# Performance work log

Hardware: AMD Instinct MI355X
Metric: run time of the kernel (lower is better)

Reference implementation:

```python
import jax, jax.numpy as jnp
import numpy as np


def setup_inputs() -> dict:
    key = jax.random.key(0)
    ks = jax.random.split(key, 12)
    B, S, D, HS, O = 512, 128, 128, 256, 1
    stdv = 1.0 / np.sqrt(HS)
    u = lambda k, shp: jax.random.uniform(k, shp, jnp.float32, -stdv, stdv)
    return {
        "H": jax.random.normal(ks[0], (B, S, D), jnp.float32),
        "y0": jax.random.normal(ks[1], (B, O), jnp.float32),
        "Wa": u(ks[2], (D, S)),
        "Ua": u(ks[3], (HS, S)),
        "ba": u(ks[4], (S,)),
        "Va": u(ks[5], (S, S)),
        "W": u(ks[6], (D, 4 * HS)),
        "U": u(ks[7], (HS, 4 * HS)),
        "bias": u(ks[8], (4 * HS,)),
        "Wy": u(ks[9], (O, 4 * HS)),
        "fc_W": u(ks[10], (O, HS)),
        "fc_b": u(ks[11], (O,)),
    }


def reference(H, y0, Wa, Ua, ba, Va, W, U, bias, Wy, fc_W, fc_b):
    B, S, D = H.shape
    HS = U.shape[0]
    # s_t in the original is initialized to zeros and never updated, so the
    # s_t @ Ua term is a constant zero; kept explicitly for faithfulness.
    s0 = jnp.zeros((B, HS), H.dtype)
    sUa = s0 @ Ua  # [B, S], zeros
    h0 = jnp.zeros((B, HS), H.dtype)
    c0 = jnp.zeros((B, HS), H.dtype)

    def step(carry, h_t):  # h_t: [B, D] = H[:, t, :]
        h_prev, c_prev, y_prev = carry
        logits = jnp.tanh(h_t @ Wa + sUa + ba) @ Va          # [B, S]
        beta = jax.nn.softmax(logits, axis=1)                # [B, S]
        pooled = jnp.einsum('bs,bsd->bd', beta, H)           # attention pool over full seq
        gates = pooled @ W + h_prev @ U + y_prev @ Wy + bias # [B, 4*HS]
        i_t, f_t, g_t, o_t = jnp.split(gates, 4, axis=1)
        c_new = jax.nn.sigmoid(f_t) * c_prev + jax.nn.sigmoid(i_t) * jnp.tanh(g_t)
        h_new = jax.nn.sigmoid(o_t) * jnp.tanh(c_new)
        y_new = h_new @ fc_W.T + fc_b                        # [B, O]
        return (h_new, c_new, y_new), h_new

    xs = jnp.transpose(H, (1, 0, 2))  # [S, B, D]
    (h_f, c_f, y_f), seq = jax.lax.scan(step, (h0, c0, y0), xs)
    hidden_seq = jnp.transpose(seq, (1, 0, 2))  # [B, S, HS]
    return y_f, hidden_seq
```

## Files before the change

### kernel.cpp

```cpp
#include <hip/hip_runtime.h>
#include <hip/hip_bf16.h>


using bf16x8 = __attribute__((ext_vector_type(8))) short;
using f32x4  = __attribute__((ext_vector_type(4))) float;

#define DEV static __device__ __forceinline__

DEV unsigned short f2bf(float x) {
    unsigned u = __float_as_uint(x);
    u += 0x7fffu + ((u >> 16) & 1u);
    return (unsigned short)(u >> 16);
}
DEV float bf2f(unsigned short s) { return __uint_as_float(((unsigned)s) << 16); }
DEV float sigm(float x) { return 1.0f / (1.0f + __expf(-x)); }
DEV float tanh_f(float x) { float e = __expf(2.0f * x); return 1.0f - 2.0f / (e + 1.0f); }
DEV f32x4 mfma16(bf16x8 a, bf16x8 b, f32x4 c) {
    return __builtin_amdgcn_mfma_f32_16x16x32_bf16(a, b, c, 0, 0, 0);
}

DEV void stage128(const unsigned short* __restrict__ src, unsigned short* dst, int rows, int tid) {
    int chunks = rows * 16;
    for (int i = tid; i < chunks; i += 256) {
        int r = i >> 4, c = (i & 15) << 3;
        *(bf16x8*)(dst + r * 136 + c) = *(const bf16x8*)(src + r * 128 + c);
    }
}
DEV void stage128f(const float* __restrict__ src, unsigned short* dst, int rows, int tid) {
    int chunks = rows * 16;
    for (int i = tid; i < chunks; i += 256) {
        int r = i >> 4, c = (i & 15) << 3;
        const float* s = src + r * 128 + c;
        bf16x8 o;
        #pragma unroll
        for (int e = 0; e < 8; ++e) o[e] = (short)f2bf(s[e]);
        *(bf16x8*)(dst + r * 136 + c) = o;
    }
}

__global__ void k_prepw(const float* __restrict__ Wa, const float* __restrict__ Va,
                        const float* __restrict__ W, const float* __restrict__ U,
                        const float* __restrict__ fcW, const float* __restrict__ Wy,
                        unsigned short* __restrict__ WaT, unsigned short* __restrict__ VaT,
                        unsigned short* __restrict__ WT, unsigned short* __restrict__ Upk) {
    int idx = blockIdx.x * 256 + threadIdx.x;
    if (idx < 16384) {
        int n = idx >> 7, k = idx & 127;
        WaT[idx] = f2bf(Wa[k * 128 + n]);
    } else if (idx < 32768) {
        int i = idx - 16384;
        int n = i >> 7, k = i & 127;
        VaT[i] = f2bf(Va[k * 128 + n]);
    } else if (idx < 163840) {
        int i = idx - 32768;
        int n = i >> 7, k = i & 127;
        WT[i] = f2bf(W[k * 1024 + n]);
    } else if (idx < 425984) {
        int i = idx - 163840;
        int j = i & 7, ll = (i >> 3) & 63, tt = (i >> 9) & 7, kc = (i >> 12) & 7, w = i >> 15;
        int k = kc * 32 + (ll >> 4) * 8 + j;
        int n = (tt >> 1) * 256 + w * 32 + (tt & 1) * 16 + (ll & 15);
        Upk[i] = f2bf(U[k * 1024 + n] + fcW[k] * Wy[n]);
    }
}

__global__ __launch_bounds__(256) void k_prept(const float* __restrict__ H,
                                               unsigned short* __restrict__ HT) {
    __shared__ unsigned short tl[128 * 130];
    int b = blockIdx.x, tid = threadIdx.x;
    const float* Hb = H + (size_t)b * 16384;
    for (int i = tid; i < 16384; i += 256) {
        int s = i >> 7, d = i & 127;
        tl[s * 130 + d] = f2bf(Hb[i]);
    }
    __syncthreads();
    unsigned short* HTb = HT + (size_t)b * 16384;
    for (int i = tid; i < 16384; i += 256) {
        int d = i >> 7, s = i & 127;
        HTb[i] = tl[s * 130 + d];
    }
}

__global__ __launch_bounds__(256) void k_att(const float* __restrict__ H,
                                             const unsigned short* __restrict__ WaT,
                                             const unsigned short* __restrict__ VaT,
                                             const unsigned short* __restrict__ HT,
                                             const float* __restrict__ ba,
                                             unsigned short* __restrict__ poolT) {
    __shared__ unsigned short A1[128 * 136];
    __shared__ unsigned short B1[128 * 136];
    int tid = threadIdx.x, b = blockIdx.x;
    int w = tid >> 6, l = tid & 63, q = l >> 4, r = l & 15;

    stage128f(H + (size_t)b * 16384, A1, 128, tid);
    stage128(WaT, B1, 128, tid);
    __syncthreads();
    f32x4 acc[2][8] = {};
    #pragma unroll
    for (int kc = 0; kc < 4; ++kc)
        #pragma unroll
        for (int mt = 0; mt < 2; ++mt) {
            bf16x8 a = *(const bf16x8*)(A1 + (w * 32 + mt * 16 + r) * 136 + kc * 32 + q * 8);
            #pragma unroll
            for (int nt = 0; nt < 8; ++nt) {
                bf16x8 bb = *(const bf16x8*)(B1 + (nt * 16 + r) * 136 + kc * 32 + q * 8);
                acc[mt][nt] = mfma16(a, bb, acc[mt][nt]);
            }
        }
    __syncthreads();
    #pragma unroll
    for (int nt = 0; nt < 8; ++nt) {
        float bav = ba[nt * 16 + r];
        #pragma unroll
        for (int mt = 0; mt < 2; ++mt)
            #pragma unroll
            for (int j = 0; j < 4; ++j)
                B1[(w * 32 + mt * 16 + q * 4 + j) * 136 + nt * 16 + r] =
                    f2bf(tanh_f(acc[mt][nt][j] + bav));
    }
    stage128(VaT, A1, 128, tid);
    __syncthreads();

    f32x4 lacc[2][8] = {};
    #pragma unroll
    for (int kc = 0; kc < 4; ++kc)
        #pragma unroll
        for (int mt = 0; mt < 2; ++mt) {
            bf16x8 a = *(const bf16x8*)(B1 + (w * 32 + mt * 16 + r) * 136 + kc * 32 + q * 8);
            #pragma unroll
            for (int nt = 0; nt < 8; ++nt) {
                bf16x8 bb = *(const bf16x8*)(A1 + (nt * 16 + r) * 136 + kc * 32 + q * 8);
                lacc[mt][nt] = mfma16(a, bb, lacc[mt][nt]);
            }
        }
    float inv_[2][4];
    #pragma unroll
    for (int mt = 0; mt < 2; ++mt)
        #pragma unroll
        for (int j = 0; j < 4; ++j) {
            float mx = lacc[mt][0][j];
            #pragma unroll
            for (int nt = 1; nt < 8; ++nt) mx = fmaxf(mx, lacc[mt][nt][j]);
            mx = fmaxf(mx, __shfl_xor(mx, 1));
            mx = fmaxf(mx, __shfl_xor(mx, 2));
            mx = fmaxf(mx, __shfl_xor(mx, 4));
            mx = fmaxf(mx, __shfl_xor(mx, 8));
            float s = 0.f;
            #pragma unroll
            for (int nt = 0; nt < 8; ++nt) {
                float e = __expf(lacc[mt][nt][j] - mx);
                lacc[mt][nt][j] = e;
                s += e;
            }
            s += __shfl_xor(s, 1);
            s += __shfl_xor(s, 2);
            s += __shfl_xor(s, 4);
            s += __shfl_xor(s, 8);
            inv_[mt][j] = 1.0f / s;
        }
    __syncthreads();
    #pragma unroll
    for (int mt = 0; mt < 2; ++mt)
        #pragma unroll
        for (int nt = 0; nt < 8; ++nt)
            #pragma unroll
            for (int j = 0; j < 4; ++j)
                B1[(w * 32 + mt * 16 + q * 4 + j) * 136 + nt * 16 + r] =
                    f2bf(lacc[mt][nt][j] * inv_[mt][j]);
    stage128(HT + (size_t)b * 16384, A1, 128, tid);
    __syncthreads();

    f32x4 pacc[2][8] = {};
    #pragma unroll
    for (int kc = 0; kc < 4; ++kc)
        #pragma unroll
        for (int mt = 0; mt < 2; ++mt) {
            bf16x8 a = *(const bf16x8*)(B1 + (w * 32 + mt * 16 + r) * 136 + kc * 32 + q * 8);
            #pragma unroll
            for (int nt = 0; nt < 8; ++nt) {
                bf16x8 bb = *(const bf16x8*)(A1 + (nt * 16 + r) * 136 + kc * 32 + q * 8);
                pacc[mt][nt] = mfma16(a, bb, pacc[mt][nt]);
            }
        }
    unsigned short* pb = poolT + (size_t)b * 16384;
    #pragma unroll
    for (int mt = 0; mt < 2; ++mt)
        #pragma unroll
        for (int nt = 0; nt < 8; ++nt)
            #pragma unroll
            for (int j = 0; j < 4; ++j)
                pb[(w * 32 + mt * 16 + q * 4 + j) * 128 + nt * 16 + r] = f2bf(pacc[mt][nt][j]);
}

__global__ __launch_bounds__(256) void k_gx(const unsigned short* __restrict__ poolT,
                                            const unsigned short* __restrict__ WT,
                                            const float* __restrict__ bias,
                                            const float* __restrict__ Wy,
                                            const float* __restrict__ y0,
                                            const float* __restrict__ fcb,
                                            unsigned short* __restrict__ Gxp) {
    __shared__ unsigned short a_lds[64 * 136];
    __shared__ unsigned short b_lds[128 * 136];
    int tid = threadIdx.x;
    int mblk = blockIdx.x >> 3, nb = blockIdx.x & 7;
    int b = mblk >> 1, t0 = (mblk & 1) * 64, n0 = nb * 128;
    stage128(poolT + (size_t)b * 16384 + t0 * 128, a_lds, 64, tid);
    stage128(WT + (size_t)n0 * 128, b_lds, 128, tid);
    __syncthreads();
    int w = tid >> 6, l = tid & 63, q = l >> 4, r = l & 15;
    f32x4 acc[8] = {};
    #pragma unroll
    for (int kc = 0; kc < 4; ++kc) {
        bf16x8 a = *(const bf16x8*)(a_lds + (w * 16 + r) * 136 + kc * 32 + q * 8);
        #pragma unroll
        for (int nt = 0; nt < 8; ++nt) {
            bf16x8 bb = *(const bf16x8*)(b_lds + (nt * 16 + r) * 136 + kc * 32 + q * 8);
            acc[nt] = mfma16(a, bb, acc[nt]);
        }
    }
    int g = b >> 2, rg = b & 3;
    float fcb0 = fcb[0];
    float y00 = y0[b];
    #pragma unroll
    for (int nt = 0; nt < 8; ++nt) {
        int col = n0 + nt * 16 + r;
        float bv = bias[col], wv = Wy[col];
        int c = col & 255;
        int w_s = c >> 5, cbit = (c >> 4) & 1;
        int l_s = ((rg & 2) | cbit) * 16 + r;
        int gate = col >> 8;
        size_t base = (size_t)g * 524288 + (size_t)w_s * 512 + (size_t)gate * 128 +
                      l_s * 2 + (rg & 1);
        #pragma unroll
        for (int j = 0; j < 4; ++j) {
            int t = t0 + w * 16 + q * 4 + j;
            float yb = (t == 0) ? y00 : fcb0;
            Gxp[base + (size_t)t * 4096] = f2bf(acc[nt][j] + bv + yb * wv);
        }
    }
}

__global__ __launch_bounds__(512, 2) void k_seq(const unsigned short* __restrict__ Gxp,
                                                const unsigned short* __restrict__ Upk,
                                                const float* __restrict__ fcW,
                                                const float* __restrict__ fcb,
                                                float* __restrict__ out) {
    extern __shared__ __align__(16) char dynbuf[];
    unsigned short* u2   = (unsigned short*)dynbuf;
    unsigned short* h_fl = (unsigned short*)(dynbuf + 131072);
    float* scr           = (float*)(dynbuf + 136192);
    float* ypart         = (float*)(dynbuf + 152576);

    int tid = threadIdx.x;
    int g = blockIdx.x;
    int w = tid >> 6, l = tid & 63, q = l >> 4, r = l & 15;
    int rr = (r < 4) ? r : 4;
    float fc_b0 = fcb[0];

    bf16x8 u_res[5][8];
    {
        const bf16x8* up = (const bf16x8*)Upk;
        const int kcs[5] = {0, 1, 2, 5, 6};
        #pragma unroll
        for (int i = 0; i < 5; ++i)
            #pragma unroll
            for (int tt = 0; tt < 8; ++tt)
                u_res[i][tt] = up[((w * 8 + kcs[i]) * 8 + tt) * 64 + l];
    }
    #pragma unroll
    for (int kcL = 0; kcL < 2; ++kcL)
        #pragma unroll
        for (int tt = 0; tt < 8; ++tt) {
            size_t gofs = (size_t)(((w * 8 + 3 + kcL) * 8 + tt) * 64 + l) * 8;
            size_t lofs = (size_t)(((w * 2 + kcL) * 8 + tt) * 64 + l) * 8;
            *(bf16x8*)(u2 + lofs) = *(const bf16x8*)(Upk + gofs);
        }

    float fw0 = fcW[w * 32 + ((q & 1) << 4) + r];
    float c_st[2] = {}, hv_st[2] = {};

    for (int i = tid; i < 2560; i += 512) h_fl[i] = 0;
    __syncthreads();

    const unsigned short* gxp = Gxp + (size_t)g * 524288 + w * 512 + l * 2;
    const bf16x8* u7p = (const bf16x8*)Upk + (w * 8 + 7) * 512 + l;
    float* outp = out + 512 + (size_t)(g * 4 + (q & 2)) * 32768 + w * 32 + ((q & 1) << 4) + r;

    for (int t = 0; t < 128; ++t) {
        unsigned short* hp = h_fl + (t & 1) * 1280;
        unsigned short* hn = h_fl + ((t & 1) ^ 1) * 1280;

        if (t > 0) {
            outp[0] = hv_st[0];
            outp[32768] = hv_st[1];
            outp += 256;
        }

        bf16x8 u7[8];
        #pragma unroll
        for (int tt = 0; tt < 8; ++tt) u7[tt] = u7p[tt * 64];

        unsigned gxv[4];
        #pragma unroll
        for (int gp = 0; gp < 4; ++gp) gxv[gp] = *(const unsigned*)(gxp + gp * 128);

        f32x4 acc[8] = {};
        #pragma unroll
        for (int i = 0; i < 3; ++i) {
            bf16x8 a = *(const bf16x8*)(hp + ((i * 4 + q) * 5 + rr) * 8);
            #pragma unroll
            for (int tt = 0; tt < 8; ++tt) acc[tt] = mfma16(a, u_res[i][tt], acc[tt]);
        }
        #pragma unroll
        for (int kcL = 0; kcL < 2; ++kcL) {
            bf16x8 a = *(const bf16x8*)(hp + (((3 + kcL) * 4 + q) * 5 + rr) * 8);
            #pragma unroll
            for (int tt = 0; tt < 8; ++tt) {
                bf16x8 u = *(const bf16x8*)(u2 + (size_t)(((w * 2 + kcL) * 8 + tt) * 64 + l) * 8);
                acc[tt] = mfma16(a, u, acc[tt]);
            }
        }
        #pragma unroll
        for (int i = 0; i < 2; ++i) {
            bf16x8 a = *(const bf16x8*)(hp + (((5 + i) * 4 + q) * 5 + rr) * 8);
            #pragma unroll
            for (int tt = 0; tt < 8; ++tt) acc[tt] = mfma16(a, u_res[3 + i][tt], acc[tt]);
        }
        {
            bf16x8 a = *(const bf16x8*)(hp + ((7 * 4 + q) * 5 + rr) * 8);
            #pragma unroll
            for (int tt = 0; tt < 8; ++tt) acc[tt] = mfma16(a, u7[tt], acc[tt]);
        }

        if (q == 0) {
            #pragma unroll
            for (int tt = 0; tt < 8; ++tt)
                *(f32x4*)(scr + ((w * 8 + tt) * 16 + r) * 4) = acc[tt];
        }
        asm volatile("s_waitcnt lgkmcnt(0)" ::: "memory");
        __builtin_amdgcn_sched_barrier(0);
        float av[4][2];
        #pragma unroll
        for (int gp = 0; gp < 4; ++gp) {
            const float* p = scr + ((w * 8 + gp * 2 + (q & 1)) * 16 + r) * 4 + (q & 2);
            av[gp][0] = p[0];
            av[gp][1] = p[1];
        }

        float ypj[2];
        #pragma unroll
        for (int jj = 0; jj < 2; ++jj) {
            int sh = jj * 16;
            float iv = sigm(av[0][jj] + bf2f((unsigned short)(gxv[0] >> sh)));
            float fv = sigm(av[1][jj] + bf2f((unsigned short)(gxv[1] >> sh)));
            float gv = tanh_f(av[2][jj] + bf2f((unsigned short)(gxv[2] >> sh)));
            float ov = sigm(av[3][jj] + bf2f((unsigned short)(gxv[3] >> sh)));
            float c = fv * c_st[jj] + iv * gv;
            c_st[jj] = c;
            float hv = ov * tanh_f(c);
            int row = (q & 2) + jj;
            hn[((w * 4 + ((q & 1) << 1) + (r >> 3)) * 5 + row) * 8 + (r & 7)] = f2bf(hv);
            hv_st[jj] = hv;
            ypj[jj] = hv * fw0;
        }
        if (t == 127) {
            #pragma unroll
            for (int jj = 0; jj < 2; ++jj) {
                float v = ypj[jj];
                v += __shfl_xor(v, 1);
                v += __shfl_xor(v, 2);
                v += __shfl_xor(v, 4);
                v += __shfl_xor(v, 8);
                v += __shfl_xor(v, 16);
                if (r == 0 && !(q & 1)) ypart[w * 4 + (q & 2) + jj] = v;
            }
        }
        gxp += 4096;
        __syncthreads();
    }

    outp[0] = hv_st[0];
    outp[32768] = hv_st[1];

    if (tid < 4) {
        float y = fc_b0;
        #pragma unroll
        for (int ww = 0; ww < 8; ++ww) y += ypart[ww * 4 + tid];
        out[g * 4 + tid] = y;
    }
}

extern "C" void kernel_launch(void* const* d_in, const int* in_sizes, int n_in,
                              void* d_out, int out_size, void* d_ws, size_t ws_size,
                              hipStream_t stream) {
    const float* H    = (const float*)d_in[0];
    const float* y0   = (const float*)d_in[1];
    const float* Wa   = (const float*)d_in[2];
    const float* ba   = (const float*)d_in[4];
    const float* Va   = (const float*)d_in[5];
    const float* W    = (const float*)d_in[6];
    const float* U    = (const float*)d_in[7];
    const float* bias = (const float*)d_in[8];
    const float* Wy   = (const float*)d_in[9];
    const float* fcW  = (const float*)d_in[10];
    const float* fcb  = (const float*)d_in[11];
    float* out = (float*)d_out;
    char* ws = (char*)d_ws;

    unsigned short* HT    = (unsigned short*)(ws);
    unsigned short* poolT = (unsigned short*)(ws + 16777216);
    unsigned short* Gxp   = (unsigned short*)(ws + 2 * 16777216);
    unsigned short* WaT   = (unsigned short*)(ws + 2 * 16777216 + 134217728);
    unsigned short* VaT   = WaT + 16384;
    unsigned short* WT    = VaT + 16384;
    unsigned short* Upk   = WT + 131072;

    hipFuncSetAttribute((const void*)k_seq, hipFuncAttributeMaxDynamicSharedMemorySize, 152704);

    hipLaunchKernelGGL(k_prepw, dim3(1664), dim3(256), 0, stream, Wa, Va, W, U, fcW, Wy,
                       WaT, VaT, WT, Upk);
    hipLaunchKernelGGL(k_prept, dim3(512), dim3(256), 0, stream, H, HT);
    hipLaunchKernelGGL(k_att, dim3(512), dim3(256), 0, stream, H, WaT, VaT, HT, ba, poolT);
    hipLaunchKernelGGL(k_gx, dim3(8192), dim3(256), 0, stream, poolT, WT, bias, Wy, y0, fcb, Gxp);
    hipLaunchKernelGGL(k_seq, dim3(128), dim3(512), 152704, stream, Gxp, Upk, fcW, fcb, out);
}
```

Before: 517.9 us.

## Split recurrent kernel to two batch rows per block across 256 blocks

The sequential LSTM kernel now handles 2 batch rows per workgroup instead of 4, doubling the grid from 128 to 256 blocks so more CUs take part in the serial recurrence. The Gxp layout written by the gate-projection kernel is repacked so each lane loads its four gate values with one 8-byte load. The LDS h buffer and scratch shrink to match, and the per-step sync becomes a raw waitcnt plus s_barrier. Each block still issues the same MFMA count per step while using fewer of the output rows, so per-block compute efficiency falls, and every block must now load the full U matrix.

```diff
diff --git a/kernel.cpp b/kernel.cpp
--- a/kernel.cpp
+++ b/kernel.cpp
@@ -4,6 +4,8 @@
 
 using bf16x8 = __attribute__((ext_vector_type(8))) short;
 using f32x4  = __attribute__((ext_vector_type(4))) float;
+using f32x2  = __attribute__((ext_vector_type(2))) float;
+using u16x4  = __attribute__((ext_vector_type(4))) unsigned short;
 
 #define DEV static __device__ __forceinline__
 
@@ -218,7 +220,7 @@
             acc[nt] = mfma16(a, bb, acc[nt]);
         }
     }
-    int g = b >> 2, rg = b & 3;
+    int g = b >> 1, rowbit = b & 1;
     float fcb0 = fcb[0];
     float y00 = y0[b];
     #pragma unroll
@@ -226,16 +228,15 @@
         int col = n0 + nt * 16 + r;
         float bv = bias[col], wv = Wy[col];
         int c = col & 255;
-        int w_s = c >> 5, cbit = (c >> 4) & 1;
-        int l_s = ((rg & 2) | cbit) * 16 + r;
+        int w_s = c >> 5, ch = (c >> 4) & 1, r_s = c & 15;
         int gate = col >> 8;
-        size_t base = (size_t)g * 524288 + (size_t)w_s * 512 + (size_t)gate * 128 +
-                      l_s * 2 + (rg & 1);
+        int l_s = (ch * 2 + rowbit) * 16 + r_s;
+        size_t base = ((((size_t)g * 128) * 8 + w_s) * 64 + l_s) * 4 + gate;
         #pragma unroll
         for (int j = 0; j < 4; ++j) {
             int t = t0 + w * 16 + q * 4 + j;
             float yb = (t == 0) ? y00 : fcb0;
-            Gxp[base + (size_t)t * 4096] = f2bf(acc[nt][j] + bv + yb * wv);
+            Gxp[base + (size_t)t * 2048] = f2bf(acc[nt][j] + bv + yb * wv);
         }
     }
 }
@@ -248,13 +249,14 @@
     extern __shared__ __align__(16) char dynbuf[];
     unsigned short* u2   = (unsigned short*)dynbuf;
     unsigned short* h_fl = (unsigned short*)(dynbuf + 131072);
-    float* scr           = (float*)(dynbuf + 136192);
-    float* ypart         = (float*)(dynbuf + 152576);
+    float* scr           = (float*)(dynbuf + 134144);
+    float* ypart         = (float*)(dynbuf + 143360);
 
     int tid = threadIdx.x;
     int g = blockIdx.x;
     int w = tid >> 6, l = tid & 63, q = l >> 4, r = l & 15;
-    int rr = (r < 4) ? r : 4;
+    int row = q & 1, ch = q >> 1;
+    int rr = (r < 2) ? r : 2;
     float fc_b0 = fcb[0];
 
     bf16x8 u_res[5][8];
@@ -276,23 +278,24 @@
             *(bf16x8*)(u2 + lofs) = *(const bf16x8*)(Upk + gofs);
         }
 
-    float fw0 = fcW[w * 32 + ((q & 1) << 4) + r];
-    float c_st[2] = {}, hv_st[2] = {};
-
-    for (int i = tid; i < 2560; i += 512) h_fl[i] = 0;
-    __syncthreads();
-
-    const unsigned short* gxp = Gxp + (size_t)g * 524288 + w * 512 + l * 2;
+    float fw0 = fcW[w * 32 + ch * 16 + r];
+    float c_st = 0.f, hv_st = 0.f;
+
+    for (int i = tid; i < 1536; i += 512) h_fl[i] = 0;
+    __syncthreads();
+
+    const unsigned short* gxp = Gxp + ((((size_t)g * 128 * 8 + w) * 64 + l) * 4);
     const bf16x8* u7p = (const bf16x8*)Upk + (w * 8 + 7) * 512 + l;
-    float* outp = out + 512 + (size_t)(g * 4 + (q & 2)) * 32768 + w * 32 + ((q & 1) << 4) + r;
+    float* outp = out + 512 + (size_t)(g * 2 + row) * 32768 + w * 32 + ch * 16 + r;
+    float* scw = scr + (w * 16 + r) * 18;
+    const float* scrd = scw + 2 * ch + row;
 
     for (int t = 0; t < 128; ++t) {
-        unsigned short* hp = h_fl + (t & 1) * 1280;
-        unsigned short* hn = h_fl + ((t & 1) ^ 1) * 1280;
+        unsigned short* hp = h_fl + (t & 1) * 768;
+        unsigned short* hn = h_fl + ((t & 1) ^ 1) * 768;
 
         if (t > 0) {
-            outp[0] = hv_st[0];
-            outp[32768] = hv_st[1];
+            *outp = hv_st;
             outp += 256;
         }
 
@@ -300,20 +303,18 @@
         #pragma unroll
         for (int tt = 0; tt < 8; ++tt) u7[tt] = u7p[tt * 64];
 
-        unsigned gxv[4];
-        #pragma unroll
-        for (int gp = 0; gp < 4; ++gp) gxv[gp] = *(const unsigned*)(gxp + gp * 128);
+        u16x4 gxv = *(const u16x4*)gxp;
 
         f32x4 acc[8] = {};
         #pragma unroll
         for (int i = 0; i < 3; ++i) {
-            bf16x8 a = *(const bf16x8*)(hp + ((i * 4 + q) * 5 + rr) * 8);
+            bf16x8 a = *(const bf16x8*)(hp + ((i * 4 + q) * 3 + rr) * 8);
             #pragma unroll
             for (int tt = 0; tt < 8; ++tt) acc[tt] = mfma16(a, u_res[i][tt], acc[tt]);
         }
         #pragma unroll
         for (int kcL = 0; kcL < 2; ++kcL) {
-            bf16x8 a = *(const bf16x8*)(hp + (((3 + kcL) * 4 + q) * 5 + rr) * 8);
+            bf16x8 a = *(const bf16x8*)(hp + (((3 + kcL) * 4 + q) * 3 + rr) * 8);
             #pragma unroll
             for (int tt = 0; tt < 8; ++tt) {
                 bf16x8 u = *(const bf16x8*)(u2 + (size_t)(((w * 2 + kcL) * 8 + tt) * 64 + l) * 8);
@@ -322,12 +323,12 @@
         }
         #pragma unroll
         for (int i = 0; i < 2; ++i) {
-            bf16x8 a = *(const bf16x8*)(hp + (((5 + i) * 4 + q) * 5 + rr) * 8);
+            bf16x8 a = *(const bf16x8*)(hp + (((5 + i) * 4 + q) * 3 + rr) * 8);
             #pragma unroll
             for (int tt = 0; tt < 8; ++tt) acc[tt] = mfma16(a, u_res[3 + i][tt], acc[tt]);
         }
         {
-            bf16x8 a = *(const bf16x8*)(hp + ((7 * 4 + q) * 5 + rr) * 8);
+            bf16x8 a = *(const bf16x8*)(hp + ((7 * 4 + q) * 3 + rr) * 8);
             #pragma unroll
             for (int tt = 0; tt < 8; ++tt) acc[tt] = mfma16(a, u7[tt], acc[tt]);
         }
@@ -335,58 +336,46 @@
         if (q == 0) {
             #pragma unroll
             for (int tt = 0; tt < 8; ++tt)
-                *(f32x4*)(scr + ((w * 8 + tt) * 16 + r) * 4) = acc[tt];
+                *(f32x2*)(scw + tt * 2) = f32x2{acc[tt][0], acc[tt][1]};
         }
         asm volatile("s_waitcnt lgkmcnt(0)" ::: "memory");
         __builtin_amdgcn_sched_barrier(0);
-        float av[4][2];
-        #pragma unroll
-        for (int gp = 0; gp < 4; ++gp) {
-            const float* p = scr + ((w * 8 + gp * 2 + (q & 1)) * 16 + r) * 4 + (q & 2);
-            av[gp][0] = p[0];
-            av[gp][1] = p[1];
-        }
-
-        float ypj[2];
-        #pragma unroll
-        for (int jj = 0; jj < 2; ++jj) {
-            int sh = jj * 16;
-            float iv = sigm(av[0][jj] + bf2f((unsigned short)(gxv[0] >> sh)));
-            float fv = sigm(av[1][jj] + bf2f((unsigned short)(gxv[1] >> sh)));
-            float gv = tanh_f(av[2][jj] + bf2f((unsigned short)(gxv[2] >> sh)));
-            float ov = sigm(av[3][jj] + bf2f((unsigned short)(gxv[3] >> sh)));
-            float c = fv * c_st[jj] + iv * gv;
-            c_st[jj] = c;
+        float av[4];
+        #pragma unroll
+        for (int gp = 0; gp < 4; ++gp) av[gp] = scrd[gp * 4];
+
+        {
+            float iv = sigm(av[0] + bf2f(gxv[0]));
+            float fv = sigm(av[1] + bf2f(gxv[1]));
+            float gv = tanh_f(av[2] + bf2f(gxv[2]));
+            float ov = sigm(av[3] + bf2f(gxv[3]));
+            float c = fv * c_st + iv * gv;
+            c_st = c;
             float hv = ov * tanh_f(c);
-            int row = (q & 2) + jj;
-            hn[((w * 4 + ((q & 1) << 1) + (r >> 3)) * 5 + row) * 8 + (r & 7)] = f2bf(hv);
-            hv_st[jj] = hv;
-            ypj[jj] = hv * fw0;
-        }
-        if (t == 127) {
-            #pragma unroll
-            for (int jj = 0; jj < 2; ++jj) {
-                float v = ypj[jj];
+            hn[((w * 4 + ch * 2 + (r >> 3)) * 3 + row) * 8 + (r & 7)] = f2bf(hv);
+            hv_st = hv;
+            if (t == 127) {
+                float v = hv * fw0;
                 v += __shfl_xor(v, 1);
                 v += __shfl_xor(v, 2);
                 v += __shfl_xor(v, 4);
                 v += __shfl_xor(v, 8);
-                v += __shfl_xor(v, 16);
-                if (r == 0 && !(q & 1)) ypart[w * 4 + (q & 2) + jj] = v;
-            }
-        }
-        gxp += 4096;
-        __syncthreads();
-    }
-
-    outp[0] = hv_st[0];
-    outp[32768] = hv_st[1];
-
-    if (tid < 4) {
+                v += __shfl_xor(v, 32);
+                if (r == 0 && ch == 0) ypart[w * 2 + row] = v;
+            }
+        }
+        gxp += 2048;
+        asm volatile("s_waitcnt lgkmcnt(0)\n\ts_barrier" ::: "memory");
+    }
+
+    *outp = hv_st;
+
+    __syncthreads();
+    if (tid < 2) {
         float y = fc_b0;
         #pragma unroll
-        for (int ww = 0; ww < 8; ++ww) y += ypart[ww * 4 + tid];
-        out[g * 4 + tid] = y;
+        for (int ww = 0; ww < 8; ++ww) y += ypart[ww * 2 + tid];
+        out[g * 2 + tid] = y;
     }
 }
 
@@ -415,12 +404,12 @@
     unsigned short* WT    = VaT + 16384;
     unsigned short* Upk   = WT + 131072;
 
-    hipFuncSetAttribute((const void*)k_seq, hipFuncAttributeMaxDynamicSharedMemorySize, 152704);
+    hipFuncSetAttribute((const void*)k_seq, hipFuncAttributeMaxDynamicSharedMemorySize, 143424);
 
     hipLaunchKernelGGL(k_prepw, dim3(1664), dim3(256), 0, stream, Wa, Va, W, U, fcW, Wy,
                        WaT, VaT, WT, Upk);
     hipLaunchKernelGGL(k_prept, dim3(512), dim3(256), 0, stream, H, HT);
     hipLaunchKernelGGL(k_att, dim3(512), dim3(256), 0, stream, H, WaT, VaT, HT, ba, poolT);
     hipLaunchKernelGGL(k_gx, dim3(8192), dim3(256), 0, stream, poolT, WT, bias, Wy, y0, fcb, Gxp);
-    hipLaunchKernelGGL(k_seq, dim3(128), dim3(512), 152704, stream, Gxp, Upk, fcW, fcb, out);
-}
+    hipLaunchKernelGGL(k_seq, dim3(256), dim3(512), 143424, stream, Gxp, Upk, fcW, fcb, out);
+}
```

Result: slower. 575.9 us (+11.2%).

## Repack Gx layout for vectorized loads and fold it into MFMA accumulators

Applied to the files above, without the earlier changes.

The k_gx producer now writes gate preactivations in a layout where each lane of quad 0 in k_seq reads 16-byte vectors covering all gates for its columns. These are added into the MFMA accumulators before the scratch spill, which removes the per-gate bf16 adds and scattered 4-byte global loads from the serial recurrence. The scratch layout is padded to a 36-float stride so reads become 2-float vector loads, and the end-of-step __syncthreads is replaced by an explicit lgkmcnt wait plus s_barrier. In exchange, k_gx stages W in four gate slices, LDS grows slightly, and the Gx loads now land on only a quarter of the lanes.

```diff
diff --git a/kernel.cpp b/kernel.cpp
--- a/kernel.cpp
+++ b/kernel.cpp
@@ -4,6 +4,7 @@
 
 using bf16x8 = __attribute__((ext_vector_type(8))) short;
 using f32x4  = __attribute__((ext_vector_type(4))) float;
+using f32x2  = __attribute__((ext_vector_type(2))) float;
 
 #define DEV static __device__ __forceinline__
 
@@ -202,10 +203,13 @@
     __shared__ unsigned short a_lds[64 * 136];
     __shared__ unsigned short b_lds[128 * 136];
     int tid = threadIdx.x;
-    int mblk = blockIdx.x >> 3, nb = blockIdx.x & 7;
-    int b = mblk >> 1, t0 = (mblk & 1) * 64, n0 = nb * 128;
-    stage128(poolT + (size_t)b * 16384 + t0 * 128, a_lds, 64, tid);
-    stage128(WT + (size_t)n0 * 128, b_lds, 128, tid);
+    int b = blockIdx.x >> 4;
+    int thalf = (blockIdx.x >> 3) & 1;
+    int ws = blockIdx.x & 7;
+    stage128(poolT + (size_t)b * 16384 + thalf * 64 * 128, a_lds, 64, tid);
+    #pragma unroll
+    for (int gate = 0; gate < 4; ++gate)
+        stage128(WT + (size_t)(gate * 256 + ws * 32) * 128, b_lds + gate * 32 * 136, 32, tid);
     __syncthreads();
     int w = tid >> 6, l = tid & 63, q = l >> 4, r = l & 15;
     f32x4 acc[8] = {};
@@ -218,25 +222,25 @@
             acc[nt] = mfma16(a, bb, acc[nt]);
         }
     }
-    int g = b >> 2, rg = b & 3;
-    float fcb0 = fcb[0];
-    float y00 = y0[b];
+    int g = b >> 2, rw = b & 3;
+    float fcb0 = fcb[0], y00 = y0[b];
+    float bv[8], wv[8];
     #pragma unroll
     for (int nt = 0; nt < 8; ++nt) {
-        int col = n0 + nt * 16 + r;
-        float bv = bias[col], wv = Wy[col];
-        int c = col & 255;
-        int w_s = c >> 5, cbit = (c >> 4) & 1;
-        int l_s = ((rg & 2) | cbit) * 16 + r;
-        int gate = col >> 8;
-        size_t base = (size_t)g * 524288 + (size_t)w_s * 512 + (size_t)gate * 128 +
-                      l_s * 2 + (rg & 1);
-        #pragma unroll
-        for (int j = 0; j < 4; ++j) {
-            int t = t0 + w * 16 + q * 4 + j;
-            float yb = (t == 0) ? y00 : fcb0;
-            Gxp[base + (size_t)t * 4096] = f2bf(acc[nt][j] + bv + yb * wv);
-        }
+        int col = (nt >> 1) * 256 + ws * 32 + (nt & 1) * 16 + r;
+        bv[nt] = bias[col];
+        wv[nt] = Wy[col];
+    }
+    #pragma unroll
+    for (int j = 0; j < 4; ++j) {
+        int t = thalf * 64 + w * 16 + q * 4 + j;
+        float yb = (t == 0) ? y00 : fcb0;
+        bf16x8 o;
+        #pragma unroll
+        for (int nt = 0; nt < 8; ++nt)
+            o[nt] = (short)f2bf(acc[nt][j] + bv[nt] + yb * wv[nt]);
+        size_t addr = ((((size_t)g * 128 + t) * 8 + ws) * 16 + r) * 32 + rw * 8;
+        *(bf16x8*)(Gxp + addr) = o;
     }
 }
 
@@ -249,7 +253,7 @@
     unsigned short* u2   = (unsigned short*)dynbuf;
     unsigned short* h_fl = (unsigned short*)(dynbuf + 131072);
     float* scr           = (float*)(dynbuf + 136192);
-    float* ypart         = (float*)(dynbuf + 152576);
+    float* ypart         = (float*)(dynbuf + 154624);
 
     int tid = threadIdx.x;
     int g = blockIdx.x;
@@ -282,9 +286,11 @@
     for (int i = tid; i < 2560; i += 512) h_fl[i] = 0;
     __syncthreads();
 
-    const unsigned short* gxp = Gxp + (size_t)g * 524288 + w * 512 + l * 2;
+    const unsigned short* gxq = Gxp + (size_t)g * 524288 + w * 512 + r * 32;
     const bf16x8* u7p = (const bf16x8*)Upk + (w * 8 + 7) * 512 + l;
     float* outp = out + 512 + (size_t)(g * 4 + (q & 2)) * 32768 + w * 32 + ((q & 1) << 4) + r;
+    float* scw = scr + (w * 16 + r) * 36;
+    const float* scrd = scw + ((q & 1) << 2) + (q & 2);
 
     for (int t = 0; t < 128; ++t) {
         unsigned short* hp = h_fl + (t & 1) * 1280;
@@ -300,9 +306,11 @@
         #pragma unroll
         for (int tt = 0; tt < 8; ++tt) u7[tt] = u7p[tt * 64];
 
-        unsigned gxv[4];
-        #pragma unroll
-        for (int gp = 0; gp < 4; ++gp) gxv[gp] = *(const unsigned*)(gxp + gp * 128);
+        bf16x8 gxv[4];
+        if (q == 0) {
+            #pragma unroll
+            for (int j2 = 0; j2 < 4; ++j2) gxv[j2] = *(const bf16x8*)(gxq + j2 * 8);
+        }
 
         f32x4 acc[8] = {};
         #pragma unroll
@@ -335,14 +343,22 @@
         if (q == 0) {
             #pragma unroll
             for (int tt = 0; tt < 8; ++tt)
-                *(f32x4*)(scr + ((w * 8 + tt) * 16 + r) * 4) = acc[tt];
+                #pragma unroll
+                for (int j = 0; j < 4; ++j)
+                    acc[tt][j] += bf2f((unsigned short)gxv[j][tt]);
+        }
+
+        if (q == 0) {
+            #pragma unroll
+            for (int tt = 0; tt < 8; ++tt)
+                *(f32x4*)(scw + tt * 4) = acc[tt];
         }
         asm volatile("s_waitcnt lgkmcnt(0)" ::: "memory");
         __builtin_amdgcn_sched_barrier(0);
         float av[4][2];
         #pragma unroll
         for (int gp = 0; gp < 4; ++gp) {
-            const float* p = scr + ((w * 8 + gp * 2 + (q & 1)) * 16 + r) * 4 + (q & 2);
+            f32x2 p = *(const f32x2*)(scrd + gp * 8);
             av[gp][0] = p[0];
             av[gp][1] = p[1];
         }
@@ -350,11 +366,10 @@
         float ypj[2];
         #pragma unroll
         for (int jj = 0; jj < 2; ++jj) {
-            int sh = jj * 16;
-            float iv = sigm(av[0][jj] + bf2f((unsigned short)(gxv[0] >> sh)));
-            float fv = sigm(av[1][jj] + bf2f((unsigned short)(gxv[1] >> sh)));
-            float gv = tanh_f(av[2][jj] + bf2f((unsigned short)(gxv[2] >> sh)));
-            float ov = sigm(av[3][jj] + bf2f((unsigned short)(gxv[3] >> sh)));
+            float iv = sigm(av[0][jj]);
+            float fv = sigm(av[1][jj]);
+            float gv = tanh_f(av[2][jj]);
+            float ov = sigm(av[3][jj]);
             float c = fv * c_st[jj] + iv * gv;
             c_st[jj] = c;
             float hv = ov * tanh_f(c);
@@ -375,13 +390,14 @@
                 if (r == 0 && !(q & 1)) ypart[w * 4 + (q & 2) + jj] = v;
             }
         }
-        gxp += 4096;
-        __syncthreads();
+        gxq += 4096;
+        asm volatile("s_waitcnt lgkmcnt(0)\n\ts_barrier" ::: "memory");
     }
 
     outp[0] = hv_st[0];
     outp[32768] = hv_st[1];
 
+    __syncthreads();
     if (tid < 4) {
         float y = fc_b0;
         #pragma unroll
@@ -415,12 +431,12 @@
     unsigned short* WT    = VaT + 16384;
     unsigned short* Upk   = WT + 131072;
 
-    hipFuncSetAttribute((const void*)k_seq, hipFuncAttributeMaxDynamicSharedMemorySize, 152704);
+    hipFuncSetAttribute((const void*)k_seq, hipFuncAttributeMaxDynamicSharedMemorySize, 154752);
 
     hipLaunchKernelGGL(k_prepw, dim3(1664), dim3(256), 0, stream, Wa, Va, W, U, fcW, Wy,
                        WaT, VaT, WT, Upk);
     hipLaunchKernelGGL(k_prept, dim3(512), dim3(256), 0, stream, H, HT);
     hipLaunchKernelGGL(k_att, dim3(512), dim3(256), 0, stream, H, WaT, VaT, HT, ba, poolT);
     hipLaunchKernelGGL(k_gx, dim3(8192), dim3(256), 0, stream, poolT, WT, bias, Wy, y0, fcb, Gxp);
-    hipLaunchKernelGGL(k_seq, dim3(128), dim3(512), 152704, stream, Gxp, Upk, fcW, fcb, out);
-}
+    hipLaunchKernelGGL(k_seq, dim3(128), dim3(512), 154752, stream, Gxp, Upk, fcW, fcb, out);
+}
```

Result: slower. 715.4 us (+38.1%).
